# Kernel tuning notes

Hardware: AMD Instinct MI355X
Metric: run time of the kernel (lower is better)

## Reference

```python
import jax, jax.numpy as jnp
import numpy as np

HID = 1024      # hidden_size (embedding dim, GRU input)
RNN = 1024      # rnn_hidden_size
VOCAB = 50000   # max_node
STEPS = 1024    # num_steps
SOS = 0


def setup_inputs() -> dict:
    key = jax.random.key(0)
    ks = jax.random.split(key, 8)
    s = 0.02
    return {
        "inputs": jax.random.randint(ks[0], (STEPS,), 0, VOCAB),
        "z": jax.random.normal(ks[1], (RNN,), jnp.float32),
        "emb_W": jax.random.uniform(ks[2], (VOCAB, HID), jnp.float32, -0.001, 0.001),
        "out_b": jnp.full((VOCAB,), 0.01, jnp.float32),
        "h2e_W": jax.random.normal(ks[3], (HID, RNN), jnp.float32) * s,
        "h2e_b": jnp.full((HID,), 0.01, jnp.float32),
        "W_ih": jax.random.normal(ks[4], (3 * RNN, HID), jnp.float32) * s,
        "W_hh": jax.random.normal(ks[5], (3 * RNN, RNN), jnp.float32) * s,
        "b_ih": jnp.zeros((3 * RNN,), jnp.float32),
        "b_hh": jnp.zeros((3 * RNN,), jnp.float32),
    }


def reference(inputs, z, emb_W, out_b, h2e_W, h2e_b, W_ih, W_hh, b_ih, b_hh):
    R = RNN

    def gru_cell(h, x):
        gi = W_ih @ x + b_ih          # (3R,)
        gh = W_hh @ h + b_hh          # (3R,)
        r = jax.nn.sigmoid(gi[:R] + gh[:R])
        zg = jax.nn.sigmoid(gi[R:2 * R] + gh[R:2 * R])
        n = jnp.tanh(gi[2 * R:] + r * gh[2 * R:])
        return (1.0 - zg) * n + zg * h

    # teacher forcing: step i consumes token_{i-1} (SOS for i=1), target is inputs[i]
    step_tokens = jnp.concatenate([jnp.array([SOS], dtype=inputs.dtype), inputs[1:-1]])
    targets = inputs[1:]

    def step(h, tok_tgt):
        tok, tgt = tok_tgt
        x = emb_W[tok]                              # embedding lookup (HID,)
        h_new = gru_cell(h, x)                      # (RNN,)
        e = h2e_W @ h_new + h2e_b                   # (HID,)
        logp = jax.nn.log_softmax(emb_W @ e + out_b)  # tied weights, (VOCAB,)
        return h_new, (-logp[tgt], jnp.argmax(logp))

    _, (losses, preds) = jax.lax.scan(step, z, (step_tokens, targets))
    loss = jnp.sum(losses)
    outputs = jnp.zeros((1, inputs.shape[0]), dtype=jnp.int32).at[0, 1:].set(preds.astype(jnp.int32))
    return loss, outputs
```

## Files before the change

kernel.cpp:

```cpp
#include <hip/hip_runtime.h>
#include <math.h>

#define NV      50000
#define T_STEPS 1023
#define KDIM    1024
#define NCH     391
typedef unsigned long long ull;


__global__ __launch_bounds__(256) void k_gather(const int* __restrict__ inputs,
                                                const float* __restrict__ emb,
                                                float* __restrict__ X) {
  const int t = blockIdx.x;
  const int tid = threadIdx.x;
  float4 v = make_float4(0.f, 0.f, 0.f, 0.f);
  if (t < T_STEPS) {
    const int tok = (t == 0) ? 0 : inputs[t];
    v = *(const float4*)&emb[(size_t)tok * KDIM + tid * 4];
  }
  *(float4*)&X[(size_t)t * KDIM + tid * 4] = v;
}

__global__ __launch_bounds__(256) void k_gemm_ffd(const float* __restrict__ A,
                                                  const float* __restrict__ B,
                                                  const float* __restrict__ bias,
                                                  double* __restrict__ C,
                                                  int N, int K) {
  __shared__ float As[32][68];
  __shared__ float Bs[32][68];
  const int tid = threadIdx.x;
  const int bx = blockIdx.x, by = blockIdx.y;
  const int lr = tid >> 2;
  const int lk = (tid & 3) * 8;
  const float* Ap = A + (size_t)(by * 64 + lr) * K + lk;
  const float* Bp = B + (size_t)(bx * 64 + lr) * K + lk;
  const int r0 = (tid >> 4) * 4;
  const int c0 = (tid & 15) * 4;
  double acc[4][4] = {};
  for (int kc = 0; kc < K; kc += 32) {
    const float4 a0 = *(const float4*)(Ap + kc);
    const float4 a1 = *(const float4*)(Ap + kc + 4);
    const float4 b0 = *(const float4*)(Bp + kc);
    const float4 b1 = *(const float4*)(Bp + kc + 4);
    __syncthreads();
    As[lk+0][lr]=a0.x; As[lk+1][lr]=a0.y; As[lk+2][lr]=a0.z; As[lk+3][lr]=a0.w;
    As[lk+4][lr]=a1.x; As[lk+5][lr]=a1.y; As[lk+6][lr]=a1.z; As[lk+7][lr]=a1.w;
    Bs[lk+0][lr]=b0.x; Bs[lk+1][lr]=b0.y; Bs[lk+2][lr]=b0.z; Bs[lk+3][lr]=b0.w;
    Bs[lk+4][lr]=b1.x; Bs[lk+5][lr]=b1.y; Bs[lk+6][lr]=b1.z; Bs[lk+7][lr]=b1.w;
    __syncthreads();
#pragma unroll
    for (int kk = 0; kk < 32; ++kk) {
      const float4 av = *(const float4*)&As[kk][r0];
      const float4 bv = *(const float4*)&Bs[kk][c0];
      const double aa[4] = {av.x, av.y, av.z, av.w};
      const double bb[4] = {bv.x, bv.y, bv.z, bv.w};
#pragma unroll
      for (int i = 0; i < 4; ++i)
#pragma unroll
        for (int j = 0; j < 4; ++j)
          acc[i][j] = fma(aa[i], bb[j], acc[i][j]);
    }
  }
  const int row = by * 64 + r0;
  const int col = bx * 64 + c0;
#pragma unroll
  for (int i = 0; i < 4; ++i)
#pragma unroll
    for (int j = 0; j < 4; ++j)
      C[(size_t)(row + i) * N + col + j] = acc[i][j] + (double)bias[col + j];
}

__global__ __launch_bounds__(256) void k_gemm_dfd(const double* __restrict__ A,
                                                  const float* __restrict__ B,
                                                  const float* __restrict__ bias,
                                                  double* __restrict__ C,
                                                  int N, int K) {
  __shared__ double As[32][68];
  __shared__ float  Bs[32][68];
  const int tid = threadIdx.x;
  const int bx = blockIdx.x, by = blockIdx.y;
  const int lr = tid >> 2;
  const int lk = (tid & 3) * 8;
  const double* Ap = A + (size_t)(by * 64 + lr) * K + lk;
  const float*  Bp = B + (size_t)(bx * 64 + lr) * K + lk;
  const int r0 = (tid >> 4) * 4;
  const int c0 = (tid & 15) * 4;
  double acc[4][4] = {};
  for (int kc = 0; kc < K; kc += 32) {
    double ar[8];
#pragma unroll
    for (int q = 0; q < 8; ++q) ar[q] = Ap[kc + q];
    const float4 b0 = *(const float4*)(Bp + kc);
    const float4 b1 = *(const float4*)(Bp + kc + 4);
    __syncthreads();
#pragma unroll
    for (int q = 0; q < 8; ++q) As[lk + q][lr] = ar[q];
    Bs[lk+0][lr]=b0.x; Bs[lk+1][lr]=b0.y; Bs[lk+2][lr]=b0.z; Bs[lk+3][lr]=b0.w;
    Bs[lk+4][lr]=b1.x; Bs[lk+5][lr]=b1.y; Bs[lk+6][lr]=b1.z; Bs[lk+7][lr]=b1.w;
    __syncthreads();
#pragma unroll
    for (int kk = 0; kk < 32; ++kk) {
      const double aa[4] = {As[kk][r0+0], As[kk][r0+1], As[kk][r0+2], As[kk][r0+3]};
      const float4 bv = *(const float4*)&Bs[kk][c0];
      const double bb[4] = {bv.x, bv.y, bv.z, bv.w};
#pragma unroll
      for (int i = 0; i < 4; ++i)
#pragma unroll
        for (int j = 0; j < 4; ++j)
          acc[i][j] = fma(aa[i], bb[j], acc[i][j]);
    }
  }
  const int row = by * 64 + r0;
  const int col = bx * 64 + c0;
#pragma unroll
  for (int i = 0; i < 4; ++i)
#pragma unroll
    for (int j = 0; j < 4; ++j)
      C[(size_t)(row + i) * N + col + j] = acc[i][j] + (double)bias[col + j];
}

__global__ __launch_bounds__(512, 2) void k_recur(const float* __restrict__ z,
                                                  const float* __restrict__ Whh,
                                                  const float* __restrict__ bhh,
                                                  const double* __restrict__ GI,
                                                  double* __restrict__ H,
                                                  ull* SA, ull* SB, int* done) {
  __shared__ double hs[1024];
  const int tid = threadIdx.x;
  const int w = tid >> 6, l = tid & 63;
  const int ibase = blockIdx.x * 16 + w * 2;
  float wreg[6][16];
#pragma unroll
  for (int il = 0; il < 2; ++il)
#pragma unroll
    for (int g = 0; g < 3; ++g) {
      const float* wp = Whh + (size_t)(g * 1024 + ibase + il) * 1024 + l;
#pragma unroll
      for (int m = 0; m < 16; ++m) wreg[il * 3 + g][m] = wp[m * 64];
    }
  double bh[6];
#pragma unroll
  for (int il = 0; il < 2; ++il)
#pragma unroll
    for (int g = 0; g < 3; ++g) bh[il * 3 + g] = (double)bhh[g * 1024 + ibase + il];

  hs[tid]       = (double)z[tid];
  hs[tid + 512] = (double)z[tid + 512];
  double gi[6];
#pragma unroll
  for (int il = 0; il < 2; ++il)
#pragma unroll
    for (int g = 0; g < 3; ++g) gi[il * 3 + g] = GI[g * 1024 + ibase + il];
  __syncthreads();

  for (int t = 0; t < T_STEPS; ++t) {
    const bool more = (t + 1 < T_STEPS);
    const int p = t & 3;
    const bool gate = more && (t >= 4);
    int dv = 0x7FFFFFFF;
    if (gate && tid < 64)
      dv = __hip_atomic_load(done + p * 64 + tid,
                             __ATOMIC_RELAXED, __HIP_MEMORY_SCOPE_AGENT);
    double s[6] = {0.0, 0.0, 0.0, 0.0, 0.0, 0.0};
#pragma unroll
    for (int m = 0; m < 16; ++m) {
      const double hv = hs[l + 64 * m];
#pragma unroll
      for (int rr = 0; rr < 6; ++rr) s[rr] = fma((double)wreg[rr][m], hv, s[rr]);
    }
#pragma unroll
    for (int rr = 0; rr < 6; ++rr) {
      double v = s[rr];
#pragma unroll
      for (int mk = 32; mk >= 1; mk >>= 1) v += __shfl_xor(v, mk, 64);
      s[rr] = v;
    }
    double hn = 0.0;
    if (l < 2) {
      const int il = l;
      const double r  = 1.0 / (1.0 + exp(-(gi[il * 3 + 0] + s[il * 3 + 0] + bh[il * 3 + 0])));
      const double zg = 1.0 / (1.0 + exp(-(gi[il * 3 + 1] + s[il * 3 + 1] + bh[il * 3 + 1])));
      const double n  = tanh(gi[il * 3 + 2] + r * (s[il * 3 + 2] + bh[il * 3 + 2]));
      hn = (1.0 - zg) * n + zg * hs[ibase + l];
    }
    double gin[6] = {0.0, 0.0, 0.0, 0.0, 0.0, 0.0};
    if (more) {
      const double* gp = GI + (size_t)(t + 1) * 3072;
#pragma unroll
      for (int il = 0; il < 2; ++il)
#pragma unroll
        for (int g = 0; g < 3; ++g) gin[il * 3 + g] = gp[g * 1024 + ibase + il];
    }
    if (gate && tid < 64) {
      while (!__all(dv >= t - 3)) {
        __builtin_amdgcn_s_sleep(1);
        dv = __hip_atomic_load(done + p * 64 + tid,
                               __ATOMIC_RELAXED, __HIP_MEMORY_SCOPE_AGENT);
      }
    }
    __syncthreads();
    if (l < 2) {
      const int gidx = ibase + l;
      H[(size_t)t * 1024 + gidx] = hn;
      if (more) {
        const ull hb  = (ull)__double_as_longlong(hn);
        const ull tag = ((ull)(t + 1)) << 32;
        __hip_atomic_store(SA + p * 1024 + gidx, tag | (hb >> 32),
                           __ATOMIC_RELAXED, __HIP_MEMORY_SCOPE_AGENT);
        __hip_atomic_store(SB + p * 1024 + gidx, tag | (hb & 0xFFFFFFFFull),
                           __ATOMIC_RELAXED, __HIP_MEMORY_SCOPE_AGENT);
      }
    }
    if (more) {
      const ull want = (ull)(t + 1);
      ull a0, b0, a1, b1;
      while (true) {
        a0 = __hip_atomic_load(SA + p * 1024 + tid,
                               __ATOMIC_RELAXED, __HIP_MEMORY_SCOPE_AGENT);
        b0 = __hip_atomic_load(SB + p * 1024 + tid,
                               __ATOMIC_RELAXED, __HIP_MEMORY_SCOPE_AGENT);
        a1 = __hip_atomic_load(SA + p * 1024 + tid + 512,
                               __ATOMIC_RELAXED, __HIP_MEMORY_SCOPE_AGENT);
        b1 = __hip_atomic_load(SB + p * 1024 + tid + 512,
                               __ATOMIC_RELAXED, __HIP_MEMORY_SCOPE_AGENT);
        if ((a0 >> 32) >= want && (b0 >> 32) >= want &&
            (a1 >> 32) >= want && (b1 >> 32) >= want) break;
        __builtin_amdgcn_s_sleep(1);
      }
      hs[tid]       = __longlong_as_double((long long)
                        (((a0 & 0xFFFFFFFFull) << 32) | (b0 & 0xFFFFFFFFull)));
      hs[tid + 512] = __longlong_as_double((long long)
                        (((a1 & 0xFFFFFFFFull) << 32) | (b1 & 0xFFFFFFFFull)));
      __syncthreads();
      if (tid == 0)
        __hip_atomic_store(done + p * 64 + blockIdx.x, t + 1,
                           __ATOMIC_RELAXED, __HIP_MEMORY_SCOPE_AGENT);
#pragma unroll
      for (int q = 0; q < 6; ++q) gi[q] = gin[q];
    }
  }
}

__global__ __launch_bounds__(256) void k_logits(const double* __restrict__ E,
                                                const float* __restrict__ emb,
                                                const float* __restrict__ out_b,
                                                const int* __restrict__ inputs,
                                                float* __restrict__ candL,
                                                int* __restrict__ candI,
                                                float* __restrict__ Psum,
                                                float* __restrict__ Ttgt) {
  __shared__ double As[32][66];
  __shared__ float  Bs[32][132];
  const int tid = threadIdx.x;
  const int bx = blockIdx.x, by = blockIdx.y;
  const int lr = tid >> 2;
  const int lk = (tid & 3) * 8;
  const double* Ap = E + (size_t)(by * 64 + lr) * KDIM + lk;
  const int bcol = tid >> 1;
  const int bk   = (tid & 1) * 16;
  const int brow = bx * 128 + bcol;
  const float* Bp = emb + (size_t)brow * KDIM + bk;
  const bool bvalid = (brow < NV);
  const int r0 = (tid >> 4) * 4;
  const int c0 = (tid & 15) * 8;
  double acc[4][8] = {};
  for (int kc = 0; kc < KDIM; kc += 32) {
    double ar[8];
#pragma unroll
    for (int q = 0; q < 8; ++q) ar[q] = Ap[kc + q];
    float4 br[4];
#pragma unroll
    for (int q = 0; q < 4; ++q)
      br[q] = bvalid ? *(const float4*)(Bp + kc + q * 4)
                     : make_float4(0.f, 0.f, 0.f, 0.f);
    __syncthreads();
#pragma unroll
    for (int q = 0; q < 8; ++q) As[lk + q][lr] = ar[q];
#pragma unroll
    for (int q = 0; q < 4; ++q) {
      Bs[bk + q * 4 + 0][bcol] = br[q].x;
      Bs[bk + q * 4 + 1][bcol] = br[q].y;
      Bs[bk + q * 4 + 2][bcol] = br[q].z;
      Bs[bk + q * 4 + 3][bcol] = br[q].w;
    }
    __syncthreads();
#pragma unroll
    for (int kk = 0; kk < 32; ++kk) {
      const double aa[4] = {As[kk][r0+0], As[kk][r0+1], As[kk][r0+2], As[kk][r0+3]};
      const float4 bv0 = *(const float4*)&Bs[kk][c0];
      const float4 bv1 = *(const float4*)&Bs[kk][c0 + 4];
      const double bb[8] = {bv0.x, bv0.y, bv0.z, bv0.w,
                            bv1.x, bv1.y, bv1.z, bv1.w};
#pragma unroll
      for (int i = 0; i < 4; ++i)
#pragma unroll
        for (int j = 0; j < 8; ++j)
          acc[i][j] = fma(aa[i], bb[j], acc[i][j]);
    }
  }
  const int colb = bx * 128 + c0;
#pragma unroll
  for (int i = 0; i < 4; ++i) {
    const int s = by * 64 + r0 + i;
    const bool valid = (s < T_STEPS);
    const int tgt = valid ? inputs[s + 1] : -1;
    float L1 = -3e38f, L2 = -3e38f;
    int   i1 = 0x7FFFFFFF, i2 = 0x7FFFFFFF;
    float se = 0.f, tv = -INFINITY;
#pragma unroll
    for (int j = 0; j < 8; ++j) {
      const int v = colb + j;
      if (v < NV) {
        const double lgd = acc[i][j] + (double)out_b[v];
        const float L = (float)lgd;
        se += expf((float)(lgd - 0.01));
        if (v == tgt) tv = (float)lgd;
        if (L > L1 || (L == L1 && v < i1)) { L2 = L1; i2 = i1; L1 = L; i1 = v; }
        else if (L > L2 || (L == L2 && v < i2)) { L2 = L; i2 = v; }
      }
    }
#pragma unroll
    for (int mk = 1; mk <= 8; mk <<= 1) {
      const float oL1 = __shfl_xor(L1, mk, 64); const int oi1 = __shfl_xor(i1, mk, 64);
      const float oL2 = __shfl_xor(L2, mk, 64); const int oi2 = __shfl_xor(i2, mk, 64);
      if (oL1 > L1 || (oL1 == L1 && oi1 < i1)) { L2 = L1; i2 = i1; L1 = oL1; i1 = oi1; }
      else if (oL1 > L2 || (oL1 == L2 && oi1 < i2)) { L2 = oL1; i2 = oi1; }
      if (oL2 > L1 || (oL2 == L1 && oi2 < i1)) { L2 = L1; i2 = i1; L1 = oL2; i1 = oi2; }
      else if (oL2 > L2 || (oL2 == L2 && oi2 < i2)) { L2 = oL2; i2 = oi2; }
      se += __shfl_xor(se, mk, 64);
      tv = fmaxf(tv, __shfl_xor(tv, mk, 64));
    }
    if (((tid & 15) == 0) && valid) {
      const size_t p = (size_t)s * (2 * NCH) + 2 * bx;
      candL[p] = L1;     candI[p] = i1;
      candL[p + 1] = L2; candI[p + 1] = i2;
      atomicAdd(&Psum[s], se);
      if (tv > -1e30f) Ttgt[s] = tv;
    }
  }
}

__global__ __launch_bounds__(256) void k_preds(const float* __restrict__ candL,
                                               const int* __restrict__ candI,
                                               float* __restrict__ out) {
  __shared__ float sL[256];
  __shared__ int   sI[256];
  const int s = blockIdx.x;
  const int tid = threadIdx.x;
  const int n = 2 * NCH;
  const size_t base = (size_t)s * n;
  float m = -3e38f;
  for (int c = tid; c < n; c += 256) m = fmaxf(m, candL[base + c]);
  sL[tid] = m; __syncthreads();
  for (int st = 128; st > 0; st >>= 1) {
    if (tid < st) sL[tid] = fmaxf(sL[tid], sL[tid + st]);
    __syncthreads();
  }
  const float Lmax = sL[0];
  __syncthreads();
  float bq = -3e38f; int bi = 0x7FFFFFFF;
  for (int c = tid; c < n; c += 256) {
    const float L = candL[base + c];
    const int   v = candI[base + c];
    const float d = L - Lmax;
    const float q = d - 10.8125f;
    if (q > bq || (q == bq && v < bi)) { bq = q; bi = v; }
  }
  sL[tid] = bq; sI[tid] = bi; __syncthreads();
  for (int st = 128; st > 0; st >>= 1) {
    if (tid < st) {
      if (sL[tid + st] > sL[tid] ||
          (sL[tid + st] == sL[tid] && sI[tid + st] < sI[tid])) {
        sL[tid] = sL[tid + st]; sI[tid] = sI[tid + st];
      }
    }
    __syncthreads();
  }
  if (tid == 0) out[2 + s] = (float)sI[0];
}

__global__ __launch_bounds__(1024) void k_finish(const float* __restrict__ Psum,
                                                 const float* __restrict__ Ttgt,
                                                 float* __restrict__ out) {
  __shared__ double red[1024];
  const int s = threadIdx.x;
  double ls = 0.0;
  if (s < T_STEPS) ls = 0.01 + log((double)Psum[s]) - (double)Ttgt[s];
  red[s] = ls;
  __syncthreads();
  for (int st = 512; st > 0; st >>= 1) {
    if (s < st) red[s] += red[s + st];
    __syncthreads();
  }
  if (s == 0) out[0] = (float)red[0];
  if (s == 1) out[1] = 0.f;
}

extern "C" void kernel_launch(void* const* d_in, const int* in_sizes, int n_in,
                              void* d_out, int out_size, void* d_ws, size_t ws_size,
                              hipStream_t stream) {
  const int*   inputs = (const int*)  d_in[0];
  const float* z      = (const float*)d_in[1];
  const float* emb    = (const float*)d_in[2];
  const float* out_b  = (const float*)d_in[3];
  const float* h2eW   = (const float*)d_in[4];
  const float* h2eb   = (const float*)d_in[5];
  const float* Wih    = (const float*)d_in[6];
  const float* Whh    = (const float*)d_in[7];
  const float* bih    = (const float*)d_in[8];
  const float* bhh    = (const float*)d_in[9];

  char* ws8 = (char*)d_ws;
  ull*    SA   = (ull*)ws8;
  ull*    SB   = (ull*)(ws8 + 32768);
  int*    done = (int*)(ws8 + 65536);
  float*  Psum = (float*)(ws8 + 66560);
  float*  Ttgt = (float*)(ws8 + 70656);
  float*  X    = (float*)(ws8 + 81920);
  char*   GIb  = ws8 + 81920 + (4u << 20);
  double* GI   = (double*)GIb;
  double* E    = GI;
  float*  candL = (float*)(GIb + (8u << 20));
  int*    candI = (int*)  (GIb + (8u << 20) + 3211264);
  double* H    = (double*)(ws8 + 81920 + (28u << 20));
  float*  out  = (float*)d_out;

  hipMemsetAsync(ws8, 0, 81920, stream);

  k_gather<<<1024, 256, 0, stream>>>(inputs, emb, X);
  k_gemm_ffd<<<dim3(48, 16), 256, 0, stream>>>(X, Wih, bih, GI, 3072, KDIM);
  k_recur<<<64, 512, 0, stream>>>(z, Whh, bhh, GI, H, SA, SB, done);
  k_gemm_dfd<<<dim3(16, 16), 256, 0, stream>>>(H, h2eW, h2eb, E, KDIM, KDIM);
  k_logits<<<dim3(NCH, 16), 256, 0, stream>>>(E, emb, out_b, inputs,
                                              candL, candI, Psum, Ttgt);
  k_preds<<<T_STEPS, 256, 0, stream>>>(candL, candI, out);
  k_finish<<<1, 1024, 0, stream>>>(Psum, Ttgt, out);
}
```

Measured before the change: 9.260 ms.

## Drop redundant done-gate in recurrence and enlarge logits row tile to 128

The recurrent kernel no longer keeps or polls the per-block 'done' counters. Blocks cannot drift more than one step apart, because each step needs every block's previous hidden values, so the 4-slot ring cannot be overwritten early. The spin-wait on the broadcast hidden state is split into two loops, one per half of the slots. The logits GEMM now computes 128 timesteps per block with an 8x8 fp64 accumulator and a row-major padded A tile, halving the grid's y dimension. This doubles reuse of each loaded embedding tile, at the cost of higher register pressure and possibly lower occupancy.

```diff
diff --git a/kernel.cpp b/kernel.cpp
--- a/kernel.cpp
+++ b/kernel.cpp
@@ -124,7 +124,7 @@
                                                   const float* __restrict__ bhh,
                                                   const double* __restrict__ GI,
                                                   double* __restrict__ H,
-                                                  ull* SA, ull* SB, int* done) {
+                                                  ull* SA, ull* SB) {
   __shared__ double hs[1024];
   const int tid = threadIdx.x;
   const int w = tid >> 6, l = tid & 63;
@@ -156,11 +156,6 @@
   for (int t = 0; t < T_STEPS; ++t) {
     const bool more = (t + 1 < T_STEPS);
     const int p = t & 3;
-    const bool gate = more && (t >= 4);
-    int dv = 0x7FFFFFFF;
-    if (gate && tid < 64)
-      dv = __hip_atomic_load(done + p * 64 + tid,
-                             __ATOMIC_RELAXED, __HIP_MEMORY_SCOPE_AGENT);
     double s[6] = {0.0, 0.0, 0.0, 0.0, 0.0, 0.0};
 #pragma unroll
     for (int m = 0; m < 16; ++m) {
@@ -190,13 +185,6 @@
       for (int il = 0; il < 2; ++il)
 #pragma unroll
         for (int g = 0; g < 3; ++g) gin[il * 3 + g] = gp[g * 1024 + ibase + il];
-    }
-    if (gate && tid < 64) {
-      while (!__all(dv >= t - 3)) {
-        __builtin_amdgcn_s_sleep(1);
-        dv = __hip_atomic_load(done + p * 64 + tid,
-                               __ATOMIC_RELAXED, __HIP_MEMORY_SCOPE_AGENT);
-      }
     }
     __syncthreads();
     if (l < 2) {
@@ -219,12 +207,15 @@
                                __ATOMIC_RELAXED, __HIP_MEMORY_SCOPE_AGENT);
         b0 = __hip_atomic_load(SB + p * 1024 + tid,
                                __ATOMIC_RELAXED, __HIP_MEMORY_SCOPE_AGENT);
+        if ((a0 >> 32) >= want && (b0 >> 32) >= want) break;
+        __builtin_amdgcn_s_sleep(1);
+      }
+      while (true) {
         a1 = __hip_atomic_load(SA + p * 1024 + tid + 512,
                                __ATOMIC_RELAXED, __HIP_MEMORY_SCOPE_AGENT);
         b1 = __hip_atomic_load(SB + p * 1024 + tid + 512,
                                __ATOMIC_RELAXED, __HIP_MEMORY_SCOPE_AGENT);
-        if ((a0 >> 32) >= want && (b0 >> 32) >= want &&
-            (a1 >> 32) >= want && (b1 >> 32) >= want) break;
+        if ((a1 >> 32) >= want && (b1 >> 32) >= want) break;
         __builtin_amdgcn_s_sleep(1);
       }
       hs[tid]       = __longlong_as_double((long long)
@@ -232,9 +223,6 @@
       hs[tid + 512] = __longlong_as_double((long long)
                         (((a1 & 0xFFFFFFFFull) << 32) | (b1 & 0xFFFFFFFFull)));
       __syncthreads();
-      if (tid == 0)
-        __hip_atomic_store(done + p * 64 + blockIdx.x, t + 1,
-                           __ATOMIC_RELAXED, __HIP_MEMORY_SCOPE_AGENT);
 #pragma unroll
       for (int q = 0; q < 6; ++q) gi[q] = gin[q];
     }
@@ -249,25 +237,25 @@
                                                 int* __restrict__ candI,
                                                 float* __restrict__ Psum,
                                                 float* __restrict__ Ttgt) {
-  __shared__ double As[32][66];
+  __shared__ double As[128][35];
   __shared__ float  Bs[32][132];
   const int tid = threadIdx.x;
   const int bx = blockIdx.x, by = blockIdx.y;
-  const int lr = tid >> 2;
-  const int lk = (tid & 3) * 8;
-  const double* Ap = E + (size_t)(by * 64 + lr) * KDIM + lk;
+  const int arow = tid >> 1;
+  const int akk  = (tid & 1) * 16;
+  const double* Ap = E + (size_t)(by * 128 + arow) * KDIM + akk;
   const int bcol = tid >> 1;
   const int bk   = (tid & 1) * 16;
   const int brow = bx * 128 + bcol;
   const float* Bp = emb + (size_t)brow * KDIM + bk;
   const bool bvalid = (brow < NV);
-  const int r0 = (tid >> 4) * 4;
+  const int r0 = (tid >> 4) * 8;
   const int c0 = (tid & 15) * 8;
-  double acc[4][8] = {};
+  double acc[8][8] = {};
   for (int kc = 0; kc < KDIM; kc += 32) {
-    double ar[8];
-#pragma unroll
-    for (int q = 0; q < 8; ++q) ar[q] = Ap[kc + q];
+    double ar[16];
+#pragma unroll
+    for (int q = 0; q < 16; ++q) ar[q] = Ap[kc + q];
     float4 br[4];
 #pragma unroll
     for (int q = 0; q < 4; ++q)
@@ -275,7 +263,7 @@
                      : make_float4(0.f, 0.f, 0.f, 0.f);
     __syncthreads();
 #pragma unroll
-    for (int q = 0; q < 8; ++q) As[lk + q][lr] = ar[q];
+    for (int q = 0; q < 16; ++q) As[arow][akk + q] = ar[q];
 #pragma unroll
     for (int q = 0; q < 4; ++q) {
       Bs[bk + q * 4 + 0][bcol] = br[q].x;
@@ -284,15 +272,17 @@
       Bs[bk + q * 4 + 3][bcol] = br[q].w;
     }
     __syncthreads();
-#pragma unroll
+#pragma unroll 4
     for (int kk = 0; kk < 32; ++kk) {
-      const double aa[4] = {As[kk][r0+0], As[kk][r0+1], As[kk][r0+2], As[kk][r0+3]};
+      double aa[8];
+#pragma unroll
+      for (int i = 0; i < 8; ++i) aa[i] = As[r0 + i][kk];
       const float4 bv0 = *(const float4*)&Bs[kk][c0];
       const float4 bv1 = *(const float4*)&Bs[kk][c0 + 4];
       const double bb[8] = {bv0.x, bv0.y, bv0.z, bv0.w,
                             bv1.x, bv1.y, bv1.z, bv1.w};
 #pragma unroll
-      for (int i = 0; i < 4; ++i)
+      for (int i = 0; i < 8; ++i)
 #pragma unroll
         for (int j = 0; j < 8; ++j)
           acc[i][j] = fma(aa[i], bb[j], acc[i][j]);
@@ -300,8 +290,8 @@
   }
   const int colb = bx * 128 + c0;
 #pragma unroll
-  for (int i = 0; i < 4; ++i) {
-    const int s = by * 64 + r0 + i;
+  for (int i = 0; i < 8; ++i) {
+    const int s = by * 128 + r0 + i;
     const bool valid = (s < T_STEPS);
     const int tgt = valid ? inputs[s + 1] : -1;
     float L1 = -3e38f, L2 = -3e38f;
@@ -413,7 +403,6 @@
   char* ws8 = (char*)d_ws;
   ull*    SA   = (ull*)ws8;
   ull*    SB   = (ull*)(ws8 + 32768);
-  int*    done = (int*)(ws8 + 65536);
   float*  Psum = (float*)(ws8 + 66560);
   float*  Ttgt = (float*)(ws8 + 70656);
   float*  X    = (float*)(ws8 + 81920);
@@ -429,10 +418,10 @@
 
   k_gather<<<1024, 256, 0, stream>>>(inputs, emb, X);
   k_gemm_ffd<<<dim3(48, 16), 256, 0, stream>>>(X, Wih, bih, GI, 3072, KDIM);
-  k_recur<<<64, 512, 0, stream>>>(z, Whh, bhh, GI, H, SA, SB, done);
+  k_recur<<<64, 512, 0, stream>>>(z, Whh, bhh, GI, H, SA, SB);
   k_gemm_dfd<<<dim3(16, 16), 256, 0, stream>>>(H, h2eW, h2eb, E, KDIM, KDIM);
-  k_logits<<<dim3(NCH, 16), 256, 0, stream>>>(E, emb, out_b, inputs,
-                                              candL, candI, Psum, Ttgt);
+  k_logits<<<dim3(NCH, 8), 256, 0, stream>>>(E, emb, out_b, inputs,
+                                             candL, candI, Psum, Ttgt);
   k_preds<<<T_STEPS, 256, 0, stream>>>(candL, candI, out);
   k_finish<<<1, 1024, 0, stream>>>(Psum, Ttgt, out);
 }
```

After: 9.921 ms. 1.07x slower.
